# Kernel tuning notes

Hardware: AMD Instinct MI355X
Metric: run time of the kernel (lower is better)

## Reference

```python
import jax, jax.numpy as jnp
import numpy as np

N_NODES = 100000
N_EDGES = 3200000


def gcn_conv(x, W, b, src, dst, n_nodes):
    """PyG GCNConv: self-loops, symmetric D^-1/2 A D^-1/2 norm, linear, bias."""
    loop = jnp.arange(n_nodes, dtype=src.dtype)
    s = jnp.concatenate([src, loop])  # [E+N]
    d = jnp.concatenate([dst, loop])  # [E+N]
    # degree computed at destination (col), edge_weight = 1
    deg = jax.ops.segment_sum(jnp.ones_like(d, dtype=x.dtype), d,
                              num_segments=n_nodes)
    dinv = jnp.where(deg > 0, jax.lax.rsqrt(deg), 0.0)
    norm = dinv[s] * dinv[d]  # [E+N]
    h = x @ W.T  # [N, out]
    msg = h[s] * norm[:, None]  # gather + scale, [E+N, out]
    out = jax.ops.segment_sum(msg, d, num_segments=n_nodes)  # scatter-add
    return out + b


def setup_inputs() -> dict:
    key = jax.random.key(0)
    k1, k2, k3, k4 = jax.random.split(key, 4)
    x = jax.random.normal(k1, (N_NODES, 2), dtype=jnp.float32)
    edge_index = jax.random.randint(k2, (2, N_EDGES), 0, N_NODES,
                                    dtype=jnp.int64)
    # Glorot-ish init for linear weights
    W1 = jax.random.normal(k3, (64, 2), dtype=jnp.float32) * 0.5
    b1 = jnp.zeros((64,), dtype=jnp.float32)
    W2 = jax.random.normal(k4, (2, 64), dtype=jnp.float32) * 0.125
    b2 = jnp.zeros((2,), dtype=jnp.float32)
    return {"x": x, "edge_index": edge_index, "W1": W1, "b1": b1,
            "W2": W2, "b2": b2}


def reference(x, edge_index, W1, b1, W2, b2):
    src, dst = edge_index[0], edge_index[1]
    h = gcn_conv(x, W1, b1, src, dst, N_NODES)
    h = jax.nn.relu(h)
    out = gcn_conv(h, W2, b2, src, dst, N_NODES)
    return out
```

## Files before the change

kernel.cpp:

```cpp
#include <hip/hip_runtime.h>

#define N_NODES 100000
#define SHIFT 8
#define BNODES 256
#define NB 391
#define CAP 9728
#define TILE 8192
#define SB 1024


__global__ __launch_bounds__(SB, 8) void k_sort(const int* __restrict__ src,
                                                const int* __restrict__ dst,
                                                int* claim,
                                                const int* __restrict__ pz,
                                                int* sg, int e) {
    __shared__ int hist[2 * NB];
    __shared__ int rank[2 * NB];
    __shared__ int addrbase[NB];
    __shared__ int partials[16];
    __shared__ int stage[TILE];
    __shared__ unsigned short binmap[TILE];

    const int t = threadIdx.x;
    const int base = blockIdx.x * TILE;
    const int n = min(TILE, e - base);
    const int goff = (t >> 9) * NB;

    for (int i = t; i < 2 * NB; i += SB) hist[i] = 0;
    __syncthreads();

    int recs[8];
    int bins[8];
    int* myh = hist + goff;
#pragma unroll
    for (int k = 0; k < 2; ++k) {
        int idx = base + (k * SB + t) * 4;
        if (idx + 3 < e) {
            int4 s4 = *(const int4*)(src + idx);
            int4 d4 = *(const int4*)(dst + idx);
            int ss[4] = {s4.x, s4.y, s4.z, s4.w};
            int dd[4] = {d4.x, d4.y, d4.z, d4.w};
#pragma unroll
            for (int j = 0; j < 4; ++j) {
                int b = dd[j] >> SHIFT;
                bins[4 * k + j] = b;
                recs[4 * k + j] = ss[j] | ((dd[j] & (BNODES - 1)) << 17);
                atomicAdd(&myh[b], 1);
            }
        } else {
#pragma unroll
            for (int j = 0; j < 4; ++j) {
                int i2 = idx + j;
                if (i2 < e) {
                    int d = dst[i2];
                    int b = d >> SHIFT;
                    bins[4 * k + j] = b;
                    recs[4 * k + j] = src[i2] | ((d & (BNODES - 1)) << 17);
                    atomicAdd(&myh[b], 1);
                } else {
                    bins[4 * k + j] = -1;
                }
            }
        }
    }
    __syncthreads();

    int c0 = 0, c1 = 0, c = 0;
    if (t < NB) {
        c0 = hist[t];
        c1 = hist[NB + t];
        c = c0 + c1;
    }
    int vs = c;
#pragma unroll
    for (int off = 1; off < 64; off <<= 1) {
        int w = __shfl_up(vs, off, 64);
        if ((t & 63) >= off) vs += w;
    }
    if ((t & 63) == 63) partials[t >> 6] = vs;
    __syncthreads();
    int add = 0;
    for (int w = 0; w < (t >> 6); ++w) add += partials[w];
    vs += add;
    int excl = vs - c;
    const int P = *pz;
    if (t < NB) {
        rank[t] = excl;
        rank[NB + t] = excl + c0;
        int rb = c ? (atomicAdd(&claim[t], c) - P) : 0;
        addrbase[t] = t * CAP + rb - excl;
    }
    __syncthreads();

    int* myr = rank + goff;
#pragma unroll
    for (int m = 0; m < 8; ++m) {
        int b = bins[m];
        if (b >= 0) {
            int pos = atomicAdd(&myr[b], 1);
            stage[pos] = recs[m];
            binmap[pos] = (unsigned short)b;
        }
    }
    __syncthreads();

    for (int i = t; i < n; i += SB) {
        sg[addrbase[binmap[i]] + i] = stage[i];
    }
}

__global__ __launch_bounds__(1024) void k_refine(const int* __restrict__ claim,
                                                 const int* __restrict__ pz,
                                                 const int* __restrict__ sg,
                                                 const float* __restrict__ x,
                                                 int* sg2, int* packed,
                                                 float2* u) {
    __shared__ int hist[4 * BNODES];
    __shared__ int rank[4 * BNODES];
    __shared__ int partials[4];
    const int t = threadIdx.x;
    const int b = blockIdx.x;
    const int* p = sg + b * CAP;
    const int len = claim[b] - *pz;
    const int g = t >> 8;

    int4 r[3];
#pragma unroll
    for (int k = 0; k < 3; ++k) {
        int idx = 4 * t + 4096 * k;
        int4 v = make_int4(-1, -1, -1, -1);
        if (idx + 3 < len) v = *(const int4*)(p + idx);
        else if (idx < len) {
            v.x = p[idx];
            if (idx + 1 < len) v.y = p[idx + 1];
            if (idx + 2 < len) v.z = p[idx + 2];
        }
        r[k] = v;
    }
    for (int i = t; i < 4 * BNODES; i += 1024) hist[i] = 0;
    __syncthreads();
    int* myh = hist + g * BNODES;
#pragma unroll
    for (int k = 0; k < 3; ++k) {
        if (r[k].x != -1) atomicAdd(&myh[((unsigned)r[k].x) >> 17], 1);
        if (r[k].y != -1) atomicAdd(&myh[((unsigned)r[k].y) >> 17], 1);
        if (r[k].z != -1) atomicAdd(&myh[((unsigned)r[k].z) >> 17], 1);
        if (r[k].w != -1) atomicAdd(&myh[((unsigned)r[k].w) >> 17], 1);
    }
    __syncthreads();

    int c4x = 0, c4y = 0, c4z = 0, c4w = 0, tot = 0;
    if (t < BNODES) {
        c4x = hist[t];
        c4y = hist[BNODES + t];
        c4z = hist[2 * BNODES + t];
        c4w = hist[3 * BNODES + t];
        tot = (c4x + c4y) + (c4z + c4w);
    }
    int vs = tot;
#pragma unroll
    for (int off = 1; off < 64; off <<= 1) {
        int w = __shfl_up(vs, off, 64);
        if ((t & 63) >= off) vs += w;
    }
    if ((t & 63) == 63 && t < BNODES) partials[t >> 6] = vs;
    __syncthreads();
    if (t < BNODES) {
        int add = 0;
        for (int w = 0; w < (t >> 6); ++w) add += partials[w];
        vs += add;
        int excl = vs - tot;
        int run = excl;
        rank[t] = run; run += c4x;
        rank[BNODES + t] = run; run += c4y;
        rank[2 * BNODES + t] = run; run += c4z;
        rank[3 * BNODES + t] = run;
        int node = b * BNODES + t;
        if (node < N_NODES) {
            packed[node] = (b * CAP + excl) | (tot << 22);
            float dv = rsqrtf((float)(tot + 1));
            float2 xv = ((const float2*)x)[node];
            u[node] = make_float2(dv * xv.x, dv * xv.y);
        }
    }
    __syncthreads();

    int* q = sg2 + b * CAP;
    int* myr = rank + g * BNODES;
#pragma unroll
    for (int k = 0; k < 3; ++k) {
        if (r[k].x != -1) q[atomicAdd(&myr[((unsigned)r[k].x) >> 17], 1)] = r[k].x & 0x1FFFF;
        if (r[k].y != -1) q[atomicAdd(&myr[((unsigned)r[k].y) >> 17], 1)] = r[k].y & 0x1FFFF;
        if (r[k].z != -1) q[atomicAdd(&myr[((unsigned)r[k].z) >> 17], 1)] = r[k].z & 0x1FFFF;
        if (r[k].w != -1) q[atomicAdd(&myr[((unsigned)r[k].w) >> 17], 1)] = r[k].w & 0x1FFFF;
    }
}

__global__ __launch_bounds__(256) void k_agg1(const int* __restrict__ sg2,
                                              const int* __restrict__ packed,
                                              const float2* __restrict__ u,
                                              const float* __restrict__ W1,
                                              const float* __restrict__ b1,
                                              const float* __restrict__ W2,
                                              float2* v) {
    __shared__ float sW1[128], sb1[64], sW2[128];
    int t = threadIdx.x;
    if (t < 128) { sW1[t] = W1[t]; sW2[t] = W2[t]; }
    else if (t < 192) sb1[t - 128] = b1[t - 128];
    __syncthreads();
    int n = blockIdx.x * 64 + (t >> 2);
    if (n >= N_NODES) return;
    int g = t & 3;
    int pk = packed[n];
    int s = pk & 0x3FFFFF;
    int cnt = ((unsigned)pk) >> 22;
    int e2 = s + cnt;
    float sx = 0.f, sy = 0.f;
    int i = s + g;
    for (; i + 12 < e2; i += 16) {
        float2 ga = u[sg2[i]];
        float2 gb = u[sg2[i + 4]];
        float2 gc = u[sg2[i + 8]];
        float2 gd = u[sg2[i + 12]];
        sx += (ga.x + gb.x) + (gc.x + gd.x);
        sy += (ga.y + gb.y) + (gc.y + gd.y);
    }
    for (; i + 4 < e2; i += 8) {
        float2 ga = u[sg2[i]];
        float2 gb = u[sg2[i + 4]];
        sx += ga.x + gb.x;
        sy += ga.y + gb.y;
    }
    if (i < e2) { float2 ga = u[sg2[i]]; sx += ga.x; sy += ga.y; }
    sx += __shfl_xor(sx, 1, 4); sy += __shfl_xor(sy, 1, 4);
    sx += __shfl_xor(sx, 2, 4); sy += __shfl_xor(sy, 2, 4);
    float dv = rsqrtf((float)(cnt + 1));
    float2 un = u[n];
    float a0 = dv * (sx + un.x), a1 = dv * (sy + un.y);
    float y0 = 0.f, y1 = 0.f;
#pragma unroll
    for (int k = 0; k < 16; ++k) {
        int j = g + 4 * k;
        float h = fmaxf(fmaf(sW1[2 * j], a0,
                        fmaf(sW1[2 * j + 1], a1, sb1[j])), 0.f);
        y0 = fmaf(sW2[j], h, y0);
        y1 = fmaf(sW2[64 + j], h, y1);
    }
    y0 += __shfl_xor(y0, 1, 4); y1 += __shfl_xor(y1, 1, 4);
    y0 += __shfl_xor(y0, 2, 4); y1 += __shfl_xor(y1, 2, 4);
    if (g == 0) v[n] = make_float2(dv * y0, dv * y1);
}

__global__ __launch_bounds__(256) void k_agg2(const int* __restrict__ sg2,
                                              const int* __restrict__ packed,
                                              const float2* __restrict__ v,
                                              const float* __restrict__ b2,
                                              float2* out) {
    int t = threadIdx.x;
    int n = blockIdx.x * 64 + (t >> 2);
    if (n >= N_NODES) return;
    int g = t & 3;
    int pk = packed[n];
    int s = pk & 0x3FFFFF;
    int cnt = ((unsigned)pk) >> 22;
    int e2 = s + cnt;
    float sx = 0.f, sy = 0.f;
    int i = s + g;
    for (; i + 12 < e2; i += 16) {
        float2 ga = v[sg2[i]];
        float2 gb = v[sg2[i + 4]];
        float2 gc = v[sg2[i + 8]];
        float2 gd = v[sg2[i + 12]];
        sx += (ga.x + gb.x) + (gc.x + gd.x);
        sy += (ga.y + gb.y) + (gc.y + gd.y);
    }
    for (; i + 4 < e2; i += 8) {
        float2 ga = v[sg2[i]];
        float2 gb = v[sg2[i + 4]];
        sx += ga.x + gb.x;
        sy += ga.y + gb.y;
    }
    if (i < e2) { float2 ga = v[sg2[i]]; sx += ga.x; sy += ga.y; }
    sx += __shfl_xor(sx, 1, 4); sy += __shfl_xor(sy, 1, 4);
    sx += __shfl_xor(sx, 2, 4); sy += __shfl_xor(sy, 2, 4);
    if (g == 0) {
        float dv = rsqrtf((float)(cnt + 1));
        float2 vn = v[n];
        out[n] = make_float2(fmaf(dv, sx + vn.x, b2[0]),
                             fmaf(dv, sy + vn.y, b2[1]));
    }
}

extern "C" void kernel_launch(void* const* d_in, const int* in_sizes, int n_in,
                              void* d_out, int out_size, void* d_ws, size_t ws_size,
                              hipStream_t stream) {
    const float* x  = (const float*)d_in[0];
    const int* ei   = (const int*)d_in[1];
    const float* W1 = (const float*)d_in[2];
    const float* b1 = (const float*)d_in[3];
    const float* W2 = (const float*)d_in[4];
    const float* b2 = (const float*)d_in[5];

    int e = in_sizes[1] / 2;
    const int* src = ei;
    const int* dst = ei + e;

    int* ws      = (int*)d_ws;
    int* claim   = ws;
    int* pz      = ws + NB;
    int* sg      = ws + 392;
    int* sg2     = sg + NB * CAP;
    int* packed  = sg2 + NB * CAP;
    float2* u    = (float2*)(packed + N_NODES);
    float2* v    = u + N_NODES;
    float2* outp = (float2*)d_out;

    const int gA = (N_NODES + 63) / 64;
    k_sort  <<<(e + TILE - 1) / TILE, SB, 0, stream>>>(src, dst, claim, pz, sg, e);
    k_refine<<<NB, 1024, 0, stream>>>(claim, pz, sg, x, sg2, packed, u);
    k_agg1  <<<gA, 256, 0, stream>>>(sg2, packed, u, W1, b1, W2, v);
    k_agg2  <<<gA, 256, 0, stream>>>(sg2, packed, v, b2, outp);
}
```

Baseline: 151.1 us.

## Fuse refine and both aggregation passes into one persistent kernel with grid barriers

Merges the per-bucket refine sort and both GCN aggregation layers into a single kernel. Each block keeps its sorted neighbor list in shared memory, and the layers are separated by software grid barriers built on global atomic counters. Buckets shrink to 128 nodes so 782 blocks can all be resident at once. This removes the sg2 and packed global round trips and two kernel launches. In exchange the barriers spin-wait and need every block to be co-resident to avoid deadlock, and the large shared-memory footprint limits occupancy.

```diff
diff --git a/kernel.cpp b/kernel.cpp
--- a/kernel.cpp
+++ b/kernel.cpp
@@ -1,10 +1,10 @@
 #include <hip/hip_runtime.h>
 
 #define N_NODES 100000
-#define SHIFT 8
-#define BNODES 256
-#define NB 391
-#define CAP 9728
+#define SHIFT 7
+#define BNODES 128
+#define NB 782
+#define CAP 5120
 #define TILE 8192
 #define SB 1024
 
@@ -109,35 +109,63 @@
     }
 }
 
-__global__ __launch_bounds__(1024) void k_refine(const int* __restrict__ claim,
-                                                 const int* __restrict__ pz,
-                                                 const int* __restrict__ sg,
-                                                 const float* __restrict__ x,
-                                                 int* sg2, int* packed,
-                                                 float2* u) {
+__device__ __forceinline__ void gbar(int* ctr, int P) {
+    __syncthreads();
+    if (threadIdx.x == 0) {
+        __threadfence();
+        __hip_atomic_fetch_add(ctr, 1, __ATOMIC_RELEASE,
+                               __HIP_MEMORY_SCOPE_AGENT);
+        while (__hip_atomic_load(ctr, __ATOMIC_ACQUIRE,
+                                 __HIP_MEMORY_SCOPE_AGENT) - P < NB) {
+            __builtin_amdgcn_s_sleep(8);
+        }
+        __threadfence();
+    }
+    __syncthreads();
+}
+
+__global__ __launch_bounds__(512, 4) void k_fused(
+        const int* __restrict__ claim, const int* __restrict__ pz,
+        const int* __restrict__ sg, const float* __restrict__ x,
+        const float* __restrict__ W1, const float* __restrict__ b1,
+        const float* __restrict__ W2, const float* __restrict__ b2v,
+        float2* __restrict__ u, float2* __restrict__ v,
+        float2* __restrict__ out, int* bar1, int* bar2) {
     __shared__ int hist[4 * BNODES];
     __shared__ int rank[4 * BNODES];
-    __shared__ int partials[4];
+    __shared__ int partials[2];
+    __shared__ int s2[CAP];
+    __shared__ int nodebeg[BNODES];
+    __shared__ int nodecnt[BNODES];
+    __shared__ float dinvl[BNODES];
+    __shared__ float uselfx[BNODES], uselfy[BNODES];
+    __shared__ float vselfx[BNODES], vselfy[BNODES];
+    __shared__ float sW1[128], sb1[64], sW2[128];
+
     const int t = threadIdx.x;
     const int b = blockIdx.x;
     const int* p = sg + b * CAP;
-    const int len = claim[b] - *pz;
-    const int g = t >> 8;
+    const int P = *pz;
+    const int len = claim[b] - P;
+    const int g = t >> 7;
+
+    if (t < 128) { sW1[t] = W1[t]; sW2[t] = W2[t]; }
+    else if (t < 192) sb1[t - 128] = b1[t - 128];
 
     int4 r[3];
 #pragma unroll
     for (int k = 0; k < 3; ++k) {
-        int idx = 4 * t + 4096 * k;
-        int4 v = make_int4(-1, -1, -1, -1);
-        if (idx + 3 < len) v = *(const int4*)(p + idx);
+        int idx = 4 * t + 2048 * k;
+        int4 vv = make_int4(-1, -1, -1, -1);
+        if (idx + 3 < len) vv = *(const int4*)(p + idx);
         else if (idx < len) {
-            v.x = p[idx];
-            if (idx + 1 < len) v.y = p[idx + 1];
-            if (idx + 2 < len) v.z = p[idx + 2];
-        }
-        r[k] = v;
-    }
-    for (int i = t; i < 4 * BNODES; i += 1024) hist[i] = 0;
+            vv.x = p[idx];
+            if (idx + 1 < len) vv.y = p[idx + 1];
+            if (idx + 2 < len) vv.z = p[idx + 2];
+        }
+        r[k] = vv;
+    }
+    for (int i = t; i < 4 * BNODES; i += 512) hist[i] = 0;
     __syncthreads();
     int* myh = hist + g * BNODES;
 #pragma unroll
@@ -175,119 +203,102 @@
         rank[BNODES + t] = run; run += c4y;
         rank[2 * BNODES + t] = run; run += c4z;
         rank[3 * BNODES + t] = run;
+        nodebeg[t] = excl;
+        nodecnt[t] = tot;
+        float dv = rsqrtf((float)(tot + 1));
+        dinvl[t] = dv;
         int node = b * BNODES + t;
         if (node < N_NODES) {
-            packed[node] = (b * CAP + excl) | (tot << 22);
-            float dv = rsqrtf((float)(tot + 1));
             float2 xv = ((const float2*)x)[node];
-            u[node] = make_float2(dv * xv.x, dv * xv.y);
-        }
-    }
-    __syncthreads();
-
-    int* q = sg2 + b * CAP;
+            float ux = dv * xv.x, uy = dv * xv.y;
+            uselfx[t] = ux; uselfy[t] = uy;
+            u[node] = make_float2(ux, uy);
+        } else { uselfx[t] = 0.f; uselfy[t] = 0.f; }
+    }
+    __syncthreads();
+
     int* myr = rank + g * BNODES;
 #pragma unroll
     for (int k = 0; k < 3; ++k) {
-        if (r[k].x != -1) q[atomicAdd(&myr[((unsigned)r[k].x) >> 17], 1)] = r[k].x & 0x1FFFF;
-        if (r[k].y != -1) q[atomicAdd(&myr[((unsigned)r[k].y) >> 17], 1)] = r[k].y & 0x1FFFF;
-        if (r[k].z != -1) q[atomicAdd(&myr[((unsigned)r[k].z) >> 17], 1)] = r[k].z & 0x1FFFF;
-        if (r[k].w != -1) q[atomicAdd(&myr[((unsigned)r[k].w) >> 17], 1)] = r[k].w & 0x1FFFF;
-    }
-}
-
-__global__ __launch_bounds__(256) void k_agg1(const int* __restrict__ sg2,
-                                              const int* __restrict__ packed,
-                                              const float2* __restrict__ u,
-                                              const float* __restrict__ W1,
-                                              const float* __restrict__ b1,
-                                              const float* __restrict__ W2,
-                                              float2* v) {
-    __shared__ float sW1[128], sb1[64], sW2[128];
-    int t = threadIdx.x;
-    if (t < 128) { sW1[t] = W1[t]; sW2[t] = W2[t]; }
-    else if (t < 192) sb1[t - 128] = b1[t - 128];
-    __syncthreads();
-    int n = blockIdx.x * 64 + (t >> 2);
-    if (n >= N_NODES) return;
-    int g = t & 3;
-    int pk = packed[n];
-    int s = pk & 0x3FFFFF;
-    int cnt = ((unsigned)pk) >> 22;
-    int e2 = s + cnt;
-    float sx = 0.f, sy = 0.f;
-    int i = s + g;
-    for (; i + 12 < e2; i += 16) {
-        float2 ga = u[sg2[i]];
-        float2 gb = u[sg2[i + 4]];
-        float2 gc = u[sg2[i + 8]];
-        float2 gd = u[sg2[i + 12]];
-        sx += (ga.x + gb.x) + (gc.x + gd.x);
-        sy += (ga.y + gb.y) + (gc.y + gd.y);
-    }
-    for (; i + 4 < e2; i += 8) {
-        float2 ga = u[sg2[i]];
-        float2 gb = u[sg2[i + 4]];
-        sx += ga.x + gb.x;
-        sy += ga.y + gb.y;
-    }
-    if (i < e2) { float2 ga = u[sg2[i]]; sx += ga.x; sy += ga.y; }
-    sx += __shfl_xor(sx, 1, 4); sy += __shfl_xor(sy, 1, 4);
-    sx += __shfl_xor(sx, 2, 4); sy += __shfl_xor(sy, 2, 4);
-    float dv = rsqrtf((float)(cnt + 1));
-    float2 un = u[n];
-    float a0 = dv * (sx + un.x), a1 = dv * (sy + un.y);
-    float y0 = 0.f, y1 = 0.f;
-#pragma unroll
-    for (int k = 0; k < 16; ++k) {
-        int j = g + 4 * k;
-        float h = fmaxf(fmaf(sW1[2 * j], a0,
-                        fmaf(sW1[2 * j + 1], a1, sb1[j])), 0.f);
-        y0 = fmaf(sW2[j], h, y0);
-        y1 = fmaf(sW2[64 + j], h, y1);
-    }
-    y0 += __shfl_xor(y0, 1, 4); y1 += __shfl_xor(y1, 1, 4);
-    y0 += __shfl_xor(y0, 2, 4); y1 += __shfl_xor(y1, 2, 4);
-    if (g == 0) v[n] = make_float2(dv * y0, dv * y1);
-}
-
-__global__ __launch_bounds__(256) void k_agg2(const int* __restrict__ sg2,
-                                              const int* __restrict__ packed,
-                                              const float2* __restrict__ v,
-                                              const float* __restrict__ b2,
-                                              float2* out) {
-    int t = threadIdx.x;
-    int n = blockIdx.x * 64 + (t >> 2);
-    if (n >= N_NODES) return;
-    int g = t & 3;
-    int pk = packed[n];
-    int s = pk & 0x3FFFFF;
-    int cnt = ((unsigned)pk) >> 22;
-    int e2 = s + cnt;
-    float sx = 0.f, sy = 0.f;
-    int i = s + g;
-    for (; i + 12 < e2; i += 16) {
-        float2 ga = v[sg2[i]];
-        float2 gb = v[sg2[i + 4]];
-        float2 gc = v[sg2[i + 8]];
-        float2 gd = v[sg2[i + 12]];
-        sx += (ga.x + gb.x) + (gc.x + gd.x);
-        sy += (ga.y + gb.y) + (gc.y + gd.y);
-    }
-    for (; i + 4 < e2; i += 8) {
-        float2 ga = v[sg2[i]];
-        float2 gb = v[sg2[i + 4]];
-        sx += ga.x + gb.x;
-        sy += ga.y + gb.y;
-    }
-    if (i < e2) { float2 ga = v[sg2[i]]; sx += ga.x; sy += ga.y; }
-    sx += __shfl_xor(sx, 1, 4); sy += __shfl_xor(sy, 1, 4);
-    sx += __shfl_xor(sx, 2, 4); sy += __shfl_xor(sy, 2, 4);
-    if (g == 0) {
-        float dv = rsqrtf((float)(cnt + 1));
-        float2 vn = v[n];
-        out[n] = make_float2(fmaf(dv, sx + vn.x, b2[0]),
-                             fmaf(dv, sy + vn.y, b2[1]));
+        if (r[k].x != -1) s2[atomicAdd(&myr[((unsigned)r[k].x) >> 17], 1)] = r[k].x & 0x1FFFF;
+        if (r[k].y != -1) s2[atomicAdd(&myr[((unsigned)r[k].y) >> 17], 1)] = r[k].y & 0x1FFFF;
+        if (r[k].z != -1) s2[atomicAdd(&myr[((unsigned)r[k].z) >> 17], 1)] = r[k].z & 0x1FFFF;
+        if (r[k].w != -1) s2[atomicAdd(&myr[((unsigned)r[k].w) >> 17], 1)] = r[k].w & 0x1FFFF;
+    }
+    gbar(bar1, P);
+
+    const int nd = t >> 2, g4 = t & 3;
+    const int node = b * BNODES + nd;
+    const int sB = nodebeg[nd];
+    const int cnt = nodecnt[nd];
+    const float dv = dinvl[nd];
+    {
+        float sx = 0.f, sy = 0.f;
+        int i = sB + g4, e2 = sB + cnt;
+        for (; i + 12 < e2; i += 16) {
+            float2 ga = u[s2[i]];
+            float2 gb = u[s2[i + 4]];
+            float2 gc = u[s2[i + 8]];
+            float2 gd = u[s2[i + 12]];
+            sx += (ga.x + gb.x) + (gc.x + gd.x);
+            sy += (ga.y + gb.y) + (gc.y + gd.y);
+        }
+        for (; i + 4 < e2; i += 8) {
+            float2 ga = u[s2[i]];
+            float2 gb = u[s2[i + 4]];
+            sx += ga.x + gb.x;
+            sy += ga.y + gb.y;
+        }
+        if (i < e2) { float2 ga = u[s2[i]]; sx += ga.x; sy += ga.y; }
+        sx += __shfl_xor(sx, 1, 4); sy += __shfl_xor(sy, 1, 4);
+        sx += __shfl_xor(sx, 2, 4); sy += __shfl_xor(sy, 2, 4);
+        float a0 = dv * (sx + uselfx[nd]);
+        float a1 = dv * (sy + uselfy[nd]);
+        float y0 = 0.f, y1 = 0.f;
+#pragma unroll
+        for (int k = 0; k < 16; ++k) {
+            int j = g4 + 4 * k;
+            float h = fmaxf(fmaf(sW1[2 * j], a0,
+                            fmaf(sW1[2 * j + 1], a1, sb1[j])), 0.f);
+            y0 = fmaf(sW2[j], h, y0);
+            y1 = fmaf(sW2[64 + j], h, y1);
+        }
+        y0 += __shfl_xor(y0, 1, 4); y1 += __shfl_xor(y1, 1, 4);
+        y0 += __shfl_xor(y0, 2, 4); y1 += __shfl_xor(y1, 2, 4);
+        if (g4 == 0) {
+            if (node < N_NODES) {
+                float vx = dv * y0, vy = dv * y1;
+                vselfx[nd] = vx; vselfy[nd] = vy;
+                v[node] = make_float2(vx, vy);
+            } else { vselfx[nd] = 0.f; vselfy[nd] = 0.f; }
+        }
+    }
+    gbar(bar2, P);
+
+    {
+        float sx = 0.f, sy = 0.f;
+        int i = sB + g4, e2 = sB + cnt;
+        for (; i + 12 < e2; i += 16) {
+            float2 ga = v[s2[i]];
+            float2 gb = v[s2[i + 4]];
+            float2 gc = v[s2[i + 8]];
+            float2 gd = v[s2[i + 12]];
+            sx += (ga.x + gb.x) + (gc.x + gd.x);
+            sy += (ga.y + gb.y) + (gc.y + gd.y);
+        }
+        for (; i + 4 < e2; i += 8) {
+            float2 ga = v[s2[i]];
+            float2 gb = v[s2[i + 4]];
+            sx += ga.x + gb.x;
+            sy += ga.y + gb.y;
+        }
+        if (i < e2) { float2 ga = v[s2[i]]; sx += ga.x; sy += ga.y; }
+        sx += __shfl_xor(sx, 1, 4); sy += __shfl_xor(sy, 1, 4);
+        sx += __shfl_xor(sx, 2, 4); sy += __shfl_xor(sy, 2, 4);
+        if (g4 == 0 && node < N_NODES) {
+            out[node] = make_float2(fmaf(dv, sx + vselfx[nd], b2v[0]),
+                                    fmaf(dv, sy + vselfy[nd], b2v[1]));
+        }
     }
 }
 
@@ -308,16 +319,14 @@
     int* ws      = (int*)d_ws;
     int* claim   = ws;
     int* pz      = ws + NB;
-    int* sg      = ws + 392;
-    int* sg2     = sg + NB * CAP;
-    int* packed  = sg2 + NB * CAP;
-    float2* u    = (float2*)(packed + N_NODES);
+    int* bar1    = ws + NB + 1;
+    int* bar2    = ws + NB + 2;
+    int* sg      = ws + 788;
+    float2* u    = (float2*)(sg + NB * CAP);
     float2* v    = u + N_NODES;
     float2* outp = (float2*)d_out;
 
-    const int gA = (N_NODES + 63) / 64;
-    k_sort  <<<(e + TILE - 1) / TILE, SB, 0, stream>>>(src, dst, claim, pz, sg, e);
-    k_refine<<<NB, 1024, 0, stream>>>(claim, pz, sg, x, sg2, packed, u);
-    k_agg1  <<<gA, 256, 0, stream>>>(sg2, packed, u, W1, b1, W2, v);
-    k_agg2  <<<gA, 256, 0, stream>>>(sg2, packed, v, b2, outp);
+    k_sort <<<(e + TILE - 1) / TILE, SB, 0, stream>>>(src, dst, claim, pz, sg, e);
+    k_fused<<<NB, 512, 0, stream>>>(claim, pz, sg, x, W1, b1, W2, b2,
+                                    u, v, outp, bar1, bar2);
 }
```

After: 425.8 us. 2.82x slower.
